# Kernel tuning notes

Hardware: AMD Instinct MI355X
Metric: run time of the kernel (lower is better)

Reference implementation:

```python
import jax, jax.numpy as jnp
import numpy as np

D_MODEL = 2048
N_HEADS = 16
D_K = D_MODEL // N_HEADS
B = 2
S = 2048


def setup_inputs() -> dict:
    key = jax.random.key(0)
    ks = jax.random.split(key, 6)
    scale = 1.0 / np.sqrt(D_MODEL)
    return {
        "inp": jax.random.normal(ks[0], (B, S, D_MODEL), dtype=jnp.float32),
        "wq": jax.random.normal(ks[1], (D_MODEL, D_MODEL), dtype=jnp.float32) * scale,
        "wk": jax.random.normal(ks[2], (D_MODEL, D_MODEL), dtype=jnp.float32) * scale,
        "wv": jax.random.normal(ks[3], (D_MODEL, D_MODEL), dtype=jnp.float32) * scale,
        "wo": jax.random.normal(ks[4], (D_MODEL, D_MODEL), dtype=jnp.float32) * scale,
        "attn_bias": jax.random.normal(ks[5], (1, 1, S, S), dtype=jnp.float32),
        "softcap": 30,
    }


def reference(inp, wq, wk, wv, wo, attn_bias, softcap):
    # inp: [B, S, D]; weights stored torch-style [out, in] -> x @ W^T
    b, s, _ = inp.shape

    def split_heads(x):  # [B,S,D] -> [B,H,S,dk]
        return x.reshape(b, s, N_HEADS, D_K).transpose(0, 2, 1, 3)

    q = split_heads(inp @ wq.T)
    k = split_heads(inp @ wk.T)
    v = split_heads(inp @ wv.T)

    scale = 1.0 / np.sqrt(D_K).astype(np.float32)
    scores = jnp.einsum("bhqd,bhkd->bhqk", q, k) * scale + attn_bias
    cap = jnp.float32(softcap)
    scores = jnp.tanh(scores / cap) * cap  # softcap > 0 branch
    weights = jax.nn.softmax(scores, axis=-1)
    o = jnp.einsum("bhqk,bhkd->bhqd", weights, v)
    o = o.transpose(0, 2, 1, 3).reshape(b, s, D_MODEL)
    return o @ wo.T
```

## Files before the change

kernel.cpp:

```cpp
#include <hip/hip_runtime.h>

#define D_MODEL 2048
#define S_LEN 2048
#define NB 2
#define NH 16
#define DK 128

typedef __attribute__((ext_vector_type(8))) __bf16 bf16x8;
typedef __attribute__((ext_vector_type(4))) float f32x4;

__device__ __forceinline__ unsigned short f2bf(float f) {
    union { __bf16 b; unsigned short u; } cv;
    cv.b = (__bf16)f;
    return cv.u;
}

__device__ __forceinline__ void gld_lds16(const void* g, void* l) {
    __builtin_amdgcn_global_load_lds(
        (const __attribute__((address_space(1))) unsigned int*)g,
        (__attribute__((address_space(3))) unsigned int*)l, 16, 0, 0);
}

__global__ void cast_f32_to_bf16(const float* __restrict__ x,
                                 unsigned short* __restrict__ y, int n4) {
    int i = blockIdx.x * blockDim.x + threadIdx.x;
    int stride = gridDim.x * blockDim.x;
    const float4* x4 = (const float4*)x;
    ushort4* y4 = (ushort4*)y;
    for (; i < n4; i += stride) {
        float4 v = x4[i];
        ushort4 o;
        o.x = f2bf(v.x); o.y = f2bf(v.y); o.z = f2bf(v.z); o.w = f2bf(v.w);
        y4[i] = o;
    }
}

__global__ void cast4_f32_to_bf16(const float* __restrict__ x0, const float* __restrict__ x1,
                                  const float* __restrict__ x2, const float* __restrict__ x3,
                                  unsigned short* y0, unsigned short* y1,
                                  unsigned short* y2, unsigned short* y3, int n4) {
    const float* x = (blockIdx.y == 0) ? x0 : (blockIdx.y == 1) ? x1 : (blockIdx.y == 2) ? x2 : x3;
    unsigned short* y = (blockIdx.y == 0) ? y0 : (blockIdx.y == 1) ? y1 : (blockIdx.y == 2) ? y2 : y3;
    int i = blockIdx.x * blockDim.x + threadIdx.x;
    int stride = gridDim.x * blockDim.x;
    const float4* x4 = (const float4*)x;
    ushort4* y4 = (ushort4*)y;
    for (; i < n4; i += stride) {
        float4 v = x4[i];
        ushort4 o;
        o.x = f2bf(v.x); o.y = f2bf(v.y); o.z = f2bf(v.z); o.w = f2bf(v.w);
        y4[i] = o;
    }
}

#define BM 128
#define BN 128
#define BK 64

__device__ __forceinline__ void cstore(float* p, float v) { *p = v; }
__device__ __forceinline__ void cstore(unsigned short* p, float v) { *p = f2bf(v); }

template <typename OutT>
__device__ __forceinline__ void gemm_body(const unsigned short* __restrict__ A,
                                          const unsigned short* __restrict__ Bt,
                                          OutT* __restrict__ C,
                                          int M, int N, int K, int m0, int n0) {
    __shared__ __align__(16) unsigned short As[BM * BK];
    __shared__ __align__(16) unsigned short Bs[BN * BK];
    const int tid = threadIdx.x;
    const int lane = tid & 63;
    const int wave = tid >> 6;
    const int quad = lane >> 4;
    const int l15 = lane & 15;
    const int wr = (wave >> 1) * 64;
    const int wc = (wave & 1) * 64;

    const int slotbase = wave * 64 + lane;

    f32x4 zero = {0.f, 0.f, 0.f, 0.f};
    f32x4 acc[4][4];
    for (int i = 0; i < 4; i++)
        for (int j = 0; j < 4; j++) acc[i][j] = zero;

    for (int k0 = 0; k0 < K; k0 += BK) {
        __syncthreads();
#pragma unroll
        for (int t = 0; t < 4; t++) {
            int slot = t * 256 + slotbase;
            int row = slot >> 3;
            int cg = (slot & 7) ^ (row & 7);
            gld_lds16(A + (size_t)(m0 + row) * K + k0 + cg * 8, &As[slot * 8]);
            gld_lds16(Bt + (size_t)(n0 + row) * K + k0 + cg * 8, &Bs[slot * 8]);
        }
        __syncthreads();

        bf16x8 af[4][2], bfr[4][2];
#pragma unroll
        for (int t = 0; t < 4; t++)
#pragma unroll
            for (int c = 0; c < 2; c++) {
                int ch = (c * 4 + quad) ^ (l15 & 7);
                af[t][c]  = *(const bf16x8*)(&As[((wr + t * 16 + l15) * 8 + ch) * 8]);
                bfr[t][c] = *(const bf16x8*)(&Bs[((wc + t * 16 + l15) * 8 + ch) * 8]);
            }
#pragma unroll
        for (int c = 0; c < 2; c++)
#pragma unroll
            for (int mt = 0; mt < 4; mt++)
#pragma unroll
                for (int nt = 0; nt < 4; nt++)
                    acc[mt][nt] = __builtin_amdgcn_mfma_f32_16x16x32_bf16(
                        af[mt][c], bfr[nt][c], acc[mt][nt], 0, 0, 0);
    }

#pragma unroll
    for (int mt = 0; mt < 4; mt++)
#pragma unroll
        for (int nt = 0; nt < 4; nt++)
#pragma unroll
            for (int r = 0; r < 4; r++) {
                int m = m0 + wr + mt * 16 + quad * 4 + r;
                int n = n0 + wc + nt * 16 + l15;
                cstore(&C[(size_t)m * N + n], acc[mt][nt][r]);
            }
}

template <typename OutT>
__global__ __launch_bounds__(256) void gemm_bt(const unsigned short* __restrict__ A,
                                               const unsigned short* __restrict__ Bt,
                                               OutT* __restrict__ C,
                                               int M, int N, int K) {
    gemm_body(A, Bt, C, M, N, K, blockIdx.x * BM, blockIdx.y * BN);
}

__global__ __launch_bounds__(256) void gemm_qk(const unsigned short* __restrict__ A,
                                               const unsigned short* __restrict__ Wq,
                                               const unsigned short* __restrict__ Wk,
                                               unsigned short* __restrict__ Qo,
                                               unsigned short* __restrict__ Ko,
                                               int M, int N, int K) {
    const int sel = blockIdx.y >> 4;
    const unsigned short* Bt = sel ? Wk : Wq;
    unsigned short* C = sel ? Ko : Qo;
    gemm_body(A, Bt, C, M, N, K, blockIdx.x * BM, (blockIdx.y & 15) * BN);
}

#define QT 128
#define PS_STRIDE 72
#define NT (S_LEN / 64)

__global__ __launch_bounds__(512, 4) void flash_attn(
        const unsigned short* __restrict__ Q,
        const unsigned short* __restrict__ K,
        const unsigned short* __restrict__ Vt,
        const float* __restrict__ bias,
        const int* __restrict__ softcap,
        unsigned short* __restrict__ O) {
    __shared__ __align__(16) unsigned short Ks[64 * DK];
    __shared__ __align__(16) unsigned short Vts[2][DK * 64];
    __shared__ __align__(16) unsigned short Ps[8 * 16 * PS_STRIDE];

    const int tid = threadIdx.x;
    const int lane = tid & 63;
    const int wave = tid >> 6;
    const int quad = lane >> 4;
    const int l15 = lane & 15;
    const int q0 = blockIdx.x * QT;
    const int h = blockIdx.y;
    const int b = blockIdx.z;

    const float scale = 0.08838834764831845f;
    const float cap = (float)softcap[0];
    const float LOG2E = 1.4426950408889634f;
    const float c1 = 2.0f * LOG2E * scale / cap;
    const float c2 = 2.0f * LOG2E / cap;
    const float c3 = -2.0f * cap * LOG2E;

    const size_t head_off = (size_t)b * S_LEN * D_MODEL + (size_t)h * DK;
    const size_t vt_row = (size_t)NB * S_LEN;
    const unsigned short* Vh = Vt + (size_t)h * DK * vt_row + (size_t)b * S_LEN;

    bf16x8 qf[4];
    {
        const unsigned short* Qp = Q + head_off + (size_t)(q0 + wave * 16 + l15) * D_MODEL;
#pragma unroll
        for (int c = 0; c < 4; c++)
            qf[c] = *(const bf16x8*)(Qp + c * 32 + quad * 8);
    }

    f32x4 zero = {0.f, 0.f, 0.f, 0.f};
    float l_part[4] = {0.f, 0.f, 0.f, 0.f};
    f32x4 o_acc[8];
#pragma unroll
    for (int d = 0; d < 8; d++) o_acc[d] = zero;

    unsigned short* Psw = &Ps[wave * 16 * PS_STRIDE];
    const int qrow = q0 + wave * 16 + quad * 4;

    auto stageK = [&](int kbase) {
#pragma unroll
        for (int t = 0; t < 2; t++) {
            int slot = t * 512 + tid;
            int kr = slot >> 4;
            int kc = (slot & 15) ^ (kr & 15);
            gld_lds16(K + head_off + (size_t)(kbase + kr) * D_MODEL + kc * 8,
                      &Ks[slot * 8]);
        }
    };
    auto stageV = [&](int kbase, int buf) {
#pragma unroll
        for (int t = 0; t < 2; t++) {
            int slot = t * 512 + tid;
            int vr = slot >> 3;
            int vc = (slot & 7) ^ (vr & 7);
            gld_lds16(Vh + (size_t)vr * vt_row + kbase + vc * 8,
                      &Vts[buf][slot * 8]);
        }
    };

    stageK(0);
    stageV(0, 0);

    for (int kt = 0; kt < NT; kt++) {
        const int kbase = kt * 64;
        __syncthreads();

        f32x4 s[4];
#pragma unroll
        for (int nt = 0; nt < 4; nt++) s[nt] = zero;
#pragma unroll
        for (int c = 0; c < 4; c++) {
            bf16x8 kf[4];
#pragma unroll
            for (int nt = 0; nt < 4; nt++)
                kf[nt] = *(const bf16x8*)(&Ks[((nt * 16 + l15) * 16 +
                                               ((c * 4 + quad) ^ l15)) * 8]);
#pragma unroll
            for (int nt = 0; nt < 4; nt++)
                s[nt] = __builtin_amdgcn_mfma_f32_16x16x32_bf16(qf[c], kf[nt], s[nt], 0, 0, 0);
        }

        __syncthreads();

        float bb[4][4];
#pragma unroll
        for (int nt = 0; nt < 4; nt++) {
            const float* bp = bias + (size_t)qrow * S_LEN + kbase + nt * 16 + l15;
#pragma unroll
            for (int r = 0; r < 4; r++)
                bb[nt][r] = bp[(size_t)r * S_LEN];
        }
        __builtin_amdgcn_sched_barrier(0);

        if (kt + 1 < NT) {
            stageK(kbase + 64);
            stageV(kbase + 64, (kt + 1) & 1);
        }

#pragma unroll
        for (int nt = 0; nt < 4; nt++) {
#pragma unroll
            for (int r = 0; r < 4; r++) {
                float arg = fmaf(s[nt][r], c1, bb[nt][r] * c2);
                float u = __builtin_amdgcn_exp2f(arg);
                float p = __builtin_amdgcn_exp2f(c3 * __builtin_amdgcn_rcpf(u + 1.0f));
                s[nt][r] = p;
                l_part[r] += p;
            }
        }

#pragma unroll
        for (int nt = 0; nt < 4; nt++)
#pragma unroll
            for (int r = 0; r < 4; r++)
                Psw[(quad * 4 + r) * PS_STRIDE + nt * 16 + l15] = f2bf(s[nt][r]);

        const unsigned short* Vcur = Vts[kt & 1];
#pragma unroll
        for (int c = 0; c < 2; c++) {
            bf16x8 pf = *(const bf16x8*)(&Psw[l15 * PS_STRIDE + c * 32 + quad * 8]);
#pragma unroll
            for (int dt = 0; dt < 8; dt++) {
                bf16x8 vf = *(const bf16x8*)(&Vcur[((dt * 16 + l15) * 8 +
                                                    ((c * 4 + quad) ^ (l15 & 7))) * 8]);
                o_acc[dt] = __builtin_amdgcn_mfma_f32_16x16x32_bf16(pf, vf, o_acc[dt], 0, 0, 0);
            }
        }
    }

#pragma unroll
    for (int r = 0; r < 4; r++) {
        float l = l_part[r];
        l += __shfl_xor(l, 1, 64);
        l += __shfl_xor(l, 2, 64);
        l += __shfl_xor(l, 4, 64);
        l += __shfl_xor(l, 8, 64);
        float inv = 1.0f / l;
        int row = qrow + r;
        unsigned short* Op = O + (size_t)(b * S_LEN + row) * D_MODEL + h * DK;
#pragma unroll
        for (int dt = 0; dt < 8; dt++)
            Op[dt * 16 + l15] = f2bf(o_acc[dt][r] * inv);
    }
}

extern "C" void kernel_launch(void* const* d_in, const int* in_sizes, int n_in,
                              void* d_out, int out_size, void* d_ws, size_t ws_size,
                              hipStream_t stream) {
    const float* inp = (const float*)d_in[0];
    const float* wq  = (const float*)d_in[1];
    const float* wk  = (const float*)d_in[2];
    const float* wv  = (const float*)d_in[3];
    const float* wo  = (const float*)d_in[4];
    const float* bias = (const float*)d_in[5];
    const int* softcap = (const int*)d_in[6];
    float* out = (float*)d_out;

    unsigned short* ws = (unsigned short*)d_ws;
    const size_t n_inp = (size_t)NB * S_LEN * D_MODEL;
    const size_t n_w = (size_t)D_MODEL * D_MODEL;
    unsigned short* inp_b = ws;
    unsigned short* wq_b = inp_b + n_inp;
    unsigned short* wk_b = wq_b + n_w;
    unsigned short* wv_b = wk_b + n_w;
    unsigned short* wo_b = wv_b + n_w;
    unsigned short* Qb = wo_b + n_w;
    unsigned short* Kb = Qb + n_inp;
    unsigned short* Vtb = Kb + n_inp;
    unsigned short* Ob = Vtb + n_inp;

    cast_f32_to_bf16<<<dim3(1024), dim3(256), 0, stream>>>(inp, inp_b, (int)(n_inp / 4));
    cast4_f32_to_bf16<<<dim3(256, 4), dim3(256), 0, stream>>>(
        wq, wk, wv, wo, wq_b, wk_b, wv_b, wo_b, (int)(n_w / 4));

    gemm_qk<<<dim3(NB * S_LEN / BM, 2 * D_MODEL / BN), 256, 0, stream>>>(
        inp_b, wq_b, wk_b, Qb, Kb, NB * S_LEN, D_MODEL, D_MODEL);
    dim3 gv(D_MODEL / BM, NB * S_LEN / BN);
    gemm_bt<unsigned short><<<gv, 256, 0, stream>>>(wv_b, inp_b, Vtb, D_MODEL, NB * S_LEN, D_MODEL);

    flash_attn<<<dim3(S_LEN / QT, NH, NB), 512, 0, stream>>>(Qb, Kb, Vtb, bias, softcap, Ob);

    dim3 gg(NB * S_LEN / BM, D_MODEL / BN);
    gemm_bt<float><<<gg, 256, 0, stream>>>(Ob, wo_b, out, NB * S_LEN, D_MODEL, D_MODEL);
}
```

Measured before the change: 438.5 us.

## Merge casts and QKV GEMMs into single launches; single-buffer V for higher occupancy

Merges the two cast kernels into one six-slice launch and the Q/K and V projection GEMMs into one 1536-block launch, cutting launch count and tail gaps. In flash attention the V tile drops from double to single buffering, freeing LDS, and launch bounds go from 4 to 6 to allow more resident blocks. V is now staged only after the PV MFMAs behind an extra barrier, so its load latency is less hidden.

```diff
diff --git a/kernel.cpp b/kernel.cpp
--- a/kernel.cpp
+++ b/kernel.cpp
@@ -21,12 +21,23 @@
         (__attribute__((address_space(3))) unsigned int*)l, 16, 0, 0);
 }
 
-__global__ void cast_f32_to_bf16(const float* __restrict__ x,
-                                 unsigned short* __restrict__ y, int n4) {
+__global__ void cast_all(const float* __restrict__ inp,
+                         const float* __restrict__ wq, const float* __restrict__ wk,
+                         const float* __restrict__ wv, const float* __restrict__ wo,
+                         unsigned short* inp_b, unsigned short* wq_b,
+                         unsigned short* wk_b, unsigned short* wv_b,
+                         unsigned short* wo_b, int n4) {
+    const int s = blockIdx.y;
+    const float4* x4;
+    ushort4* y4;
+    if (s == 0)      { x4 = (const float4*)inp;            y4 = (ushort4*)inp_b; }
+    else if (s == 1) { x4 = (const float4*)inp + n4;       y4 = (ushort4*)inp_b + n4; }
+    else if (s == 2) { x4 = (const float4*)wq;             y4 = (ushort4*)wq_b; }
+    else if (s == 3) { x4 = (const float4*)wk;             y4 = (ushort4*)wk_b; }
+    else if (s == 4) { x4 = (const float4*)wv;             y4 = (ushort4*)wv_b; }
+    else             { x4 = (const float4*)wo;             y4 = (ushort4*)wo_b; }
     int i = blockIdx.x * blockDim.x + threadIdx.x;
     int stride = gridDim.x * blockDim.x;
-    const float4* x4 = (const float4*)x;
-    ushort4* y4 = (ushort4*)y;
     for (; i < n4; i += stride) {
         float4 v = x4[i];
         ushort4 o;
@@ -35,24 +46,6 @@
     }
 }
 
-__global__ void cast4_f32_to_bf16(const float* __restrict__ x0, const float* __restrict__ x1,
-                                  const float* __restrict__ x2, const float* __restrict__ x3,
-                                  unsigned short* y0, unsigned short* y1,
-                                  unsigned short* y2, unsigned short* y3, int n4) {
-    const float* x = (blockIdx.y == 0) ? x0 : (blockIdx.y == 1) ? x1 : (blockIdx.y == 2) ? x2 : x3;
-    unsigned short* y = (blockIdx.y == 0) ? y0 : (blockIdx.y == 1) ? y1 : (blockIdx.y == 2) ? y2 : y3;
-    int i = blockIdx.x * blockDim.x + threadIdx.x;
-    int stride = gridDim.x * blockDim.x;
-    const float4* x4 = (const float4*)x;
-    ushort4* y4 = (ushort4*)y;
-    for (; i < n4; i += stride) {
-        float4 v = x4[i];
-        ushort4 o;
-        o.x = f2bf(v.x); o.y = f2bf(v.y); o.z = f2bf(v.z); o.w = f2bf(v.w);
-        y4[i] = o;
-    }
-}
-
 #define BM 128
 #define BN 128
 #define BK 64
@@ -64,7 +57,7 @@
 __device__ __forceinline__ void gemm_body(const unsigned short* __restrict__ A,
                                           const unsigned short* __restrict__ Bt,
                                           OutT* __restrict__ C,
-                                          int M, int N, int K, int m0, int n0) {
+                                          int N, int K, int m0, int n0) {
     __shared__ __align__(16) unsigned short As[BM * BK];
     __shared__ __align__(16) unsigned short Bs[BN * BK];
     const int tid = threadIdx.x;
@@ -125,31 +118,46 @@
             }
 }
 
-template <typename OutT>
-__global__ __launch_bounds__(256) void gemm_bt(const unsigned short* __restrict__ A,
-                                               const unsigned short* __restrict__ Bt,
-                                               OutT* __restrict__ C,
-                                               int M, int N, int K) {
-    gemm_body(A, Bt, C, M, N, K, blockIdx.x * BM, blockIdx.y * BN);
-}
-
-__global__ __launch_bounds__(256) void gemm_qk(const unsigned short* __restrict__ A,
-                                               const unsigned short* __restrict__ Wq,
-                                               const unsigned short* __restrict__ Wk,
-                                               unsigned short* __restrict__ Qo,
-                                               unsigned short* __restrict__ Ko,
-                                               int M, int N, int K) {
-    const int sel = blockIdx.y >> 4;
-    const unsigned short* Bt = sel ? Wk : Wq;
-    unsigned short* C = sel ? Ko : Qo;
-    gemm_body(A, Bt, C, M, N, K, blockIdx.x * BM, (blockIdx.y & 15) * BN);
+__global__ __launch_bounds__(256) void gemm_qkv(
+        const unsigned short* __restrict__ inp,
+        const unsigned short* __restrict__ wq,
+        const unsigned short* __restrict__ wk,
+        const unsigned short* __restrict__ wv,
+        unsigned short* __restrict__ Qo,
+        unsigned short* __restrict__ Ko,
+        unsigned short* __restrict__ Vto) {
+    const int bid = blockIdx.x;
+    const unsigned short *A, *Bt;
+    unsigned short* C;
+    int N, m0, n0;
+    if (bid < 1024) {
+        int sel = bid >> 9;
+        int r = bid & 511;
+        A = inp; Bt = sel ? wk : wq; C = sel ? Ko : Qo;
+        N = D_MODEL;
+        m0 = (r & 31) * BM;
+        n0 = (r >> 5) * BN;
+    } else {
+        int r = bid - 1024;
+        A = wv; Bt = inp; C = Vto;
+        N = NB * S_LEN;
+        m0 = (r & 15) * BM;
+        n0 = (r >> 4) * BN;
+    }
+    gemm_body(A, Bt, C, N, D_MODEL, m0, n0);
+}
+
+__global__ __launch_bounds__(256) void gemm_out(const unsigned short* __restrict__ A,
+                                                const unsigned short* __restrict__ Bt,
+                                                float* __restrict__ C) {
+    gemm_body(A, Bt, C, D_MODEL, D_MODEL, blockIdx.x * BM, blockIdx.y * BN);
 }
 
 #define QT 128
 #define PS_STRIDE 72
 #define NT (S_LEN / 64)
 
-__global__ __launch_bounds__(512, 4) void flash_attn(
+__global__ __launch_bounds__(512, 6) void flash_attn(
         const unsigned short* __restrict__ Q,
         const unsigned short* __restrict__ K,
         const unsigned short* __restrict__ Vt,
@@ -157,7 +165,7 @@
         const int* __restrict__ softcap,
         unsigned short* __restrict__ O) {
     __shared__ __align__(16) unsigned short Ks[64 * DK];
-    __shared__ __align__(16) unsigned short Vts[2][DK * 64];
+    __shared__ __align__(16) unsigned short Vts[DK * 64];
     __shared__ __align__(16) unsigned short Ps[8 * 16 * PS_STRIDE];
 
     const int tid = threadIdx.x;
@@ -207,19 +215,19 @@
                       &Ks[slot * 8]);
         }
     };
-    auto stageV = [&](int kbase, int buf) {
+    auto stageV = [&](int kbase) {
 #pragma unroll
         for (int t = 0; t < 2; t++) {
             int slot = t * 512 + tid;
             int vr = slot >> 3;
             int vc = (slot & 7) ^ (vr & 7);
             gld_lds16(Vh + (size_t)vr * vt_row + kbase + vc * 8,
-                      &Vts[buf][slot * 8]);
+                      &Vts[slot * 8]);
         }
     };
 
     stageK(0);
-    stageV(0, 0);
+    stageV(0);
 
     for (int kt = 0; kt < NT; kt++) {
         const int kbase = kt * 64;
@@ -252,10 +260,7 @@
         }
         __builtin_amdgcn_sched_barrier(0);
 
-        if (kt + 1 < NT) {
-            stageK(kbase + 64);
-            stageV(kbase + 64, (kt + 1) & 1);
-        }
+        if (kt + 1 < NT) stageK(kbase + 64);
 
 #pragma unroll
         for (int nt = 0; nt < 4; nt++) {
@@ -275,16 +280,20 @@
             for (int r = 0; r < 4; r++)
                 Psw[(quad * 4 + r) * PS_STRIDE + nt * 16 + l15] = f2bf(s[nt][r]);
 
-        const unsigned short* Vcur = Vts[kt & 1];
 #pragma unroll
         for (int c = 0; c < 2; c++) {
             bf16x8 pf = *(const bf16x8*)(&Psw[l15 * PS_STRIDE + c * 32 + quad * 8]);
 #pragma unroll
             for (int dt = 0; dt < 8; dt++) {
-                bf16x8 vf = *(const bf16x8*)(&Vcur[((dt * 16 + l15) * 8 +
-                                                    ((c * 4 + quad) ^ (l15 & 7))) * 8]);
+                bf16x8 vf = *(const bf16x8*)(&Vts[((dt * 16 + l15) * 8 +
+                                                   ((c * 4 + quad) ^ (l15 & 7))) * 8]);
                 o_acc[dt] = __builtin_amdgcn_mfma_f32_16x16x32_bf16(pf, vf, o_acc[dt], 0, 0, 0);
             }
+        }
+
+        if (kt + 1 < NT) {
+            __syncthreads();
+            stageV(kbase + 64);
         }
     }
 
@@ -329,17 +338,12 @@
     unsigned short* Vtb = Kb + n_inp;
     unsigned short* Ob = Vtb + n_inp;
 
-    cast_f32_to_bf16<<<dim3(1024), dim3(256), 0, stream>>>(inp, inp_b, (int)(n_inp / 4));
-    cast4_f32_to_bf16<<<dim3(256, 4), dim3(256), 0, stream>>>(
-        wq, wk, wv, wo, wq_b, wk_b, wv_b, wo_b, (int)(n_w / 4));
-
-    gemm_qk<<<dim3(NB * S_LEN / BM, 2 * D_MODEL / BN), 256, 0, stream>>>(
-        inp_b, wq_b, wk_b, Qb, Kb, NB * S_LEN, D_MODEL, D_MODEL);
-    dim3 gv(D_MODEL / BM, NB * S_LEN / BN);
-    gemm_bt<unsigned short><<<gv, 256, 0, stream>>>(wv_b, inp_b, Vtb, D_MODEL, NB * S_LEN, D_MODEL);
+    cast_all<<<dim3(256, 6), dim3(256), 0, stream>>>(
+        inp, wq, wk, wv, wo, inp_b, wq_b, wk_b, wv_b, wo_b, (int)(n_w / 4));
+
+    gemm_qkv<<<dim3(1536), 256, 0, stream>>>(inp_b, wq_b, wk_b, wv_b, Qb, Kb, Vtb);
 
     flash_attn<<<dim3(S_LEN / QT, NH, NB), 512, 0, stream>>>(Qb, Kb, Vtb, bias, softcap, Ob);
 
-    dim3 gg(NB * S_LEN / BM, D_MODEL / BN);
-    gemm_bt<float><<<gg, 256, 0, stream>>>(Ob, wo_b, out, NB * S_LEN, D_MODEL, D_MODEL);
-}
+    gemm_out<<<dim3(NB * S_LEN / BM, D_MODEL / BN), 256, 0, stream>>>(Ob, wo_b, out);
+}
```

Measured after the change: 704.9 us. +60.8%, slower.
